# Kernel optimization log

Measured on AMD Instinct MI355X. Metric: run time of the kernel, lower is better.

## Reference

```python
import jax, jax.numpy as jnp
import numpy as np

B, R, NB, T = 32, 96, 5, 2048
FEAT_DIM = 64
SPARSITY = 0.2


def _per_band(X, community, W1, b1, W2, b2):
    # X: [R, T] wavelet coeffs for one (batch, band) slice
    n, t = X.shape
    f32 = X.dtype
    # --- functional connectivity (cosine of centered signals == Pearson corr) ---
    Xc = X - X.mean(axis=1, keepdims=True)
    norm = jnp.linalg.norm(Xc, axis=1, keepdims=True)
    norm = jnp.where(norm == 0, 1.0, norm)
    C = (Xc @ Xc.T) / (norm * norm.T)
    C = jnp.nan_to_num(C, nan=0.0)
    C = C * (1.0 - jnp.eye(n, dtype=f32))  # zero diagonal
    # --- quantile sparsification over strict lower triangle ---
    ti, tj = np.tril_indices(n, -1)
    thr = jnp.quantile(jnp.abs(C[ti, tj]), 1.0 - SPARSITY)
    A = C * (jnp.abs(C) >= thr).astype(f32)  # graph_type == 'weighted'
    # --- node features (5-dim, averaged over regions) ---
    mean_f = X.mean(axis=1)
    std_f = jnp.std(X, axis=1, ddof=1)  # torch.std is unbiased
    energy_f = (X ** 2).sum(axis=1)
    maxamp_f = jnp.abs(X).max(axis=1)
    ps = jnp.abs(jnp.fft.fft(X, axis=1)) ** 2
    ps = ps[:, : t // 2]
    s = ps.sum(axis=1, keepdims=True)
    s = jnp.where(s == 0, 1.0, s)
    p = ps / s
    ent_f = -(p * jnp.log(p + 1e-10)).sum(axis=1)
    node5 = jnp.stack([mean_f, std_f, energy_f, maxamp_f, ent_f], axis=1).mean(axis=0)
    # --- graph properties (6-dim) on binarized adjacency ---
    Bm = (A != 0).astype(f32)
    ne = Bm.sum() / 2.0
    density = ne / (n * (n - 1) / 2.0)
    deg = Bm.sum(axis=1)
    avg_deg = deg.mean()
    A2 = Bm @ Bm
    tri = (A2 * Bm).sum() / 6.0
    poss = (deg * (deg - 1.0)).sum() / 2.0
    clus = jnp.where(poss > 0, tri / jnp.where(poss > 0, poss, 1.0), 0.0)
    # global efficiency: safe reciprocal (zero where A+I == 0; original would emit inf)
    denom = Bm + jnp.eye(n, dtype=f32)
    eff = jnp.where(denom > 0, 1.0 / jnp.where(denom > 0, denom, 1.0), 0.0).sum() / (n * (n - 1))
    # approximate modularity with fixed 2-community assignment (deterministic)
    m2 = 2.0 * ne
    m2_safe = jnp.where(m2 > 0, m2, 1.0)
    same = (community[:, None] == community[None, :]) & (~jnp.eye(n, dtype=bool))
    expected = jnp.outer(deg, deg) / m2_safe
    mod = jnp.where(m2 > 0, (same * (Bm - expected)).sum() / m2_safe, 0.0)
    props = jnp.stack([ne, density, avg_deg, clus, eff, mod])
    feat11 = jnp.concatenate([node5, props])  # [11]
    # --- feature encoder MLP (dropout is identity at inference) ---
    h = jnp.maximum(feat11 @ W1.T + b1, 0.0)
    return A, h @ W2.T + b2


def _forward(wavelet_coeffs, frequency_bands, community, W1, b1, W2, b2):
    b, r, nb, t = wavelet_coeffs.shape
    Xs = wavelet_coeffs.transpose(0, 2, 1, 3).reshape(b * nb, r, t)  # [B*NB, R, T]
    A, F = jax.vmap(_per_band, in_axes=(0, None, None, None, None, None))(
        Xs, community, W1, b1, W2, b2)
    return A.reshape(b, nb, r, r), F.reshape(b, nb, -1)


def setup_inputs() -> dict:
    key = jax.random.key(0)
    k0, k1, k2, k3, k4 = jax.random.split(key, 5)
    wavelet_coeffs = jax.random.normal(k0, (B, R, NB, T), dtype=jnp.float32)
    frequency_bands = jax.random.uniform(k1, (NB, 2), dtype=jnp.float32)
    community = jax.random.randint(k2, (R,), 0, 2)
    W1 = jax.random.normal(k3, (32, 11), dtype=jnp.float32) * 0.3
    b1 = jnp.zeros((32,), jnp.float32)
    W2 = jax.random.normal(k4, (FEAT_DIM, 32), dtype=jnp.float32) * 0.18
    b2 = jnp.zeros((FEAT_DIM,), jnp.float32)
    return {"wavelet_coeffs": wavelet_coeffs, "frequency_bands": frequency_bands,
            "community": community, "W1": W1, "b1": b1, "W2": W2, "b2": b2}


def reference(wavelet_coeffs, frequency_bands, community, W1, b1, W2, b2):
    return _forward(wavelet_coeffs, frequency_bands, community, W1, b1, W2, b2)
```

## Files before the change

kernel.cpp:

```cpp
#include <hip/hip_runtime.h>
#include <hip/hip_bf16.h>
#include <math.h>
#include <float.h>

#ifndef M_PI
#define M_PI 3.14159265358979323846
#endif

#define NBANDS 160
#define RR 96
#define TT 2048
#define NTRIL 4560
#define A_ELEMS ((size_t)NBANDS * RR * RR)
#define NBIN 8192
#define MAXCAND 512
#define BKS 64
#define NST (TT / BKS)
#define GPITCH 76
#define FBLK 384

#define PHI(L) ((L) ^ (((L) >> 5) & 31))

typedef float  f32x4  __attribute__((ext_vector_type(4)));
typedef __bf16 bf16x8 __attribute__((ext_vector_type(8)));
typedef __bf16 bf16x4 __attribute__((ext_vector_type(4)));

__device__ inline void blockReduceSum4(double v0, double v1, double v2, double v3,
                                       double* sred, double out[4]) {
    for (int off = 32; off > 0; off >>= 1) {
        v0 += __shfl_down(v0, off, 64);
        v1 += __shfl_down(v1, off, 64);
        v2 += __shfl_down(v2, off, 64);
        v3 += __shfl_down(v3, off, 64);
    }
    int lane = threadIdx.x & 63, wid = threadIdx.x >> 6;
    int nw = blockDim.x >> 6;
    if (lane == 0) {
        sred[wid * 4 + 0] = v0; sred[wid * 4 + 1] = v1;
        sred[wid * 4 + 2] = v2; sred[wid * 4 + 3] = v3;
    }
    __syncthreads();
    if (threadIdx.x < 4) {
        double r = sred[threadIdx.x];
        for (int w = 1; w < nw; w++) r += sred[w * 4 + threadIdx.x];
        sred[nw * 4 + threadIdx.x] = r;
    }
    __syncthreads();
    out[0] = sred[nw * 4 + 0]; out[1] = sred[nw * 4 + 1];
    out[2] = sred[nw * 4 + 2]; out[3] = sred[nw * 4 + 3];
    __syncthreads();
}

__device__ inline void blockReduceSum2(double v0, double v1,
                                       double* sred, double out[2]) {
    for (int off = 32; off > 0; off >>= 1) {
        v0 += __shfl_down(v0, off, 64);
        v1 += __shfl_down(v1, off, 64);
    }
    int lane = threadIdx.x & 63, wid = threadIdx.x >> 6;
    int nw = blockDim.x >> 6;
    if (lane == 0) { sred[wid * 2 + 0] = v0; sred[wid * 2 + 1] = v1; }
    __syncthreads();
    if (threadIdx.x < 2) {
        double r = sred[threadIdx.x];
        for (int w = 1; w < nw; w++) r += sred[w * 2 + threadIdx.x];
        sred[nw * 2 + threadIdx.x] = r;
    }
    __syncthreads();
    out[0] = sred[nw * 2 + 0]; out[1] = sred[nw * 2 + 1];
    __syncthreads();
}

__device__ inline void blockReduceMax2(double v0, double v1,
                                       double* sred, double out[2]) {
    for (int off = 32; off > 0; off >>= 1) {
        v0 = fmax(v0, __shfl_down(v0, off, 64));
        v1 = fmax(v1, __shfl_down(v1, off, 64));
    }
    int lane = threadIdx.x & 63, wid = threadIdx.x >> 6;
    int nw = blockDim.x >> 6;
    if (lane == 0) { sred[wid * 2 + 0] = v0; sred[wid * 2 + 1] = v1; }
    __syncthreads();
    if (threadIdx.x < 2) {
        double r = sred[threadIdx.x];
        for (int w = 1; w < nw; w++) r = fmax(r, sred[w * 2 + threadIdx.x]);
        sred[nw * 2 + threadIdx.x] = r;
    }
    __syncthreads();
    out[0] = sred[nw * 2 + 0]; out[1] = sred[nw * 2 + 1];
    __syncthreads();
}

__global__ void twiddle_kernel(float* tw) {
    int k = blockIdx.x * blockDim.x + threadIdx.x;
    if (k < 1024) {
        double ang = -2.0 * M_PI * (double)k / 2048.0;
        tw[2 * k]     = (float)cos(ang);
        tw[2 * k + 1] = (float)sin(ang);
    }
}

#define BFLY(r1, r2, WR, WI) do { \
    float _wr = (WR), _wi = (WI); \
    float _tr = _wr * yr[r2] - _wi * yi[r2]; \
    float _ti = _wr * yi[r2] + _wi * yr[r2]; \
    yr[r2] = yr[r1] - _tr; yi[r2] = yi[r1] - _ti; \
    yr[r1] += _tr; yi[r1] += _ti; } while (0)

__global__ __launch_bounds__(256) void rowstat_fft_kernel(
    const float* __restrict__ wc, const float* __restrict__ tw,
    double* __restrict__ rowstats)
{
    __shared__ float re[TT];
    __shared__ float im[TT];
    __shared__ double sred[32];
    __shared__ float bcast[4];

    int t = threadIdx.x;
    int g0 = blockIdx.x * 2;
    int g1 = g0 + 1;

    int band = g0 / RR, r0 = g0 % RR;
    int b = band / 5, nb = band % 5;
    size_t base0 = ((size_t)(b * RR + r0) * 5 + nb) * TT;
    size_t base1 = base0 + (size_t)5 * TT;
    const float2* twv = (const float2*)tw;

    float s0 = 0.f, s1 = 0.f, q0 = 0.f, q1 = 0.f, m0 = 0.f, m1 = 0.f;
#pragma unroll
    for (int c = 0; c < 8; c++) {
        int i = t + c * 256;
        float af = wc[base0 + i];
        float bf = wc[base1 + i];
        int P = PHI(i);
        re[P] = af; im[P] = bf;
        s0 += af; s1 += bf;
        q0 = fmaf(af, af, q0); q1 = fmaf(bf, bf, q1);
        m0 = fmaxf(m0, fabsf(af)); m1 = fmaxf(m1, fabsf(bf));
    }
    __syncthreads();

    double S4[4], M2[2];
    blockReduceSum4((double)s0, (double)s1, (double)q0, (double)q1, sred, S4);
    blockReduceMax2((double)m0, (double)m1, sred, M2);
    double SUM0 = S4[0], SUM1 = S4[1], SQ0 = S4[2], SQ1 = S4[3];
    double MX0 = M2[0], MX1 = M2[1];

    float yr[8], yi[8];

#pragma unroll
    for (int j = 0; j < 8; j++) {
        int p = 8 * t + j;
        int L = (int)(__brev((unsigned)p) >> 21);
        int P = PHI(L);
        yr[j] = re[P]; yi[j] = im[P];
    }

    const float RC = 0.70710678f;
    BFLY(0, 1, 1.0f, 0.0f); BFLY(2, 3, 1.0f, 0.0f);
    BFLY(4, 5, 1.0f, 0.0f); BFLY(6, 7, 1.0f, 0.0f);
    BFLY(0, 2, 1.0f, 0.0f); BFLY(1, 3, 0.0f, -1.0f);
    BFLY(4, 6, 1.0f, 0.0f); BFLY(5, 7, 0.0f, -1.0f);
    BFLY(0, 4, 1.0f, 0.0f); BFLY(1, 5, RC, -RC);
    BFLY(2, 6, 0.0f, -1.0f); BFLY(3, 7, -RC, -RC);

    __syncthreads();
#pragma unroll
    for (int j = 0; j < 8; j++) {
        int P = PHI(8 * t + j);
        re[P] = yr[j]; im[P] = yi[j];
    }
    __syncthreads();
    int oo = t & 7;
    int bb64 = 4 * ((t >> 3) & 7) + (t >> 6);
#pragma unroll
    for (int k = 0; k < 8; k++) {
        int P = PHI(64 * bb64 + 8 * k + oo);
        yr[k] = re[P]; yi[k] = im[P];
    }

    {
        float2 w0 = twv[oo << 7];
        BFLY(0, 1, w0.x, w0.y); BFLY(2, 3, w0.x, w0.y);
        BFLY(4, 5, w0.x, w0.y); BFLY(6, 7, w0.x, w0.y);
        float2 wa = twv[oo << 6];
        float2 wb = twv[(oo + 8) << 6];
        BFLY(0, 2, wa.x, wa.y); BFLY(1, 3, wb.x, wb.y);
        BFLY(4, 6, wa.x, wa.y); BFLY(5, 7, wb.x, wb.y);
        float2 wc0 = twv[oo << 5], wc1 = twv[(oo + 8) << 5];
        float2 wc2 = twv[(oo + 16) << 5], wc3 = twv[(oo + 24) << 5];
        BFLY(0, 4, wc0.x, wc0.y);
        BFLY(1, 5, wc1.x, wc1.y);
        BFLY(2, 6, wc2.x, wc2.y);
        BFLY(3, 7, wc3.x, wc3.y);
    }

    __syncthreads();
#pragma unroll
    for (int k = 0; k < 8; k++) {
        int P = PHI(64 * bb64 + 8 * k + oo);
        re[P] = yr[k]; im[P] = yi[k];
    }
    __syncthreads();
    int O3 = t & 63, Wq = t >> 6;
#pragma unroll
    for (int s = 0; s < 2; s++) {
        int B3 = Wq + 4 * s;
#pragma unroll
        for (int k = 0; k < 4; k++) {
            int P = PHI(256 * B3 + 64 * k + O3);
            yr[4 * s + k] = re[P]; yi[4 * s + k] = im[P];
        }
    }

    {
        float2 w0 = twv[O3 << 4];
        float2 wa = twv[O3 << 3];
        float2 wb = twv[(O3 + 64) << 3];
        BFLY(0, 1, w0.x, w0.y); BFLY(2, 3, w0.x, w0.y);
        BFLY(4, 5, w0.x, w0.y); BFLY(6, 7, w0.x, w0.y);
        BFLY(0, 2, wa.x, wa.y); BFLY(1, 3, wb.x, wb.y);
        BFLY(4, 6, wa.x, wa.y); BFLY(5, 7, wb.x, wb.y);
    }

    __syncthreads();
#pragma unroll
    for (int s = 0; s < 2; s++) {
        int B3 = Wq + 4 * s;
#pragma unroll
        for (int k = 0; k < 4; k++) {
            int P = PHI(256 * B3 + 64 * k + O3);
            re[P] = yr[4 * s + k]; im[P] = yi[4 * s + k];
        }
    }
    __syncthreads();
#pragma unroll
    for (int k = 0; k < 8; k++) {
        int P = PHI(256 * k + t);
        yr[k] = re[P]; yi[k] = im[P];
    }

    {
        float2 w0 = twv[t << 2];
        float2 wa = twv[t << 1];
        float2 wb = twv[(t + 256) << 1];
        BFLY(0, 1, w0.x, w0.y); BFLY(2, 3, w0.x, w0.y);
        BFLY(4, 5, w0.x, w0.y); BFLY(6, 7, w0.x, w0.y);
        BFLY(0, 2, wa.x, wa.y); BFLY(1, 3, wb.x, wb.y);
        BFLY(4, 6, wa.x, wa.y); BFLY(5, 7, wb.x, wb.y);
        float2 wf0 = twv[t], wf1 = twv[t + 256];
        float2 wf2 = twv[t + 512], wf3 = twv[t + 768];
        BFLY(0, 4, wf0.x, wf0.y);
        BFLY(1, 5, wf1.x, wf1.y);
        BFLY(2, 6, wf2.x, wf2.y);
        BFLY(3, 7, wf3.x, wf3.y);
    }

    __syncthreads();
#pragma unroll
    for (int k = 0; k < 8; k++) {
        int P = PHI(256 * k + t);
        re[P] = yr[k]; im[P] = yi[k];
    }
    __syncthreads();

    float psa[8], psb[8];
#pragma unroll
    for (int k = 0; k < 8; k++) {
        int q = (2048 - t - 256 * k) & 2047;
        int P = PHI(q);
        float prr = re[P], pii = im[P];
        float sr = yr[k] + prr, di = yi[k] - pii;
        float si = yi[k] + pii, dr = yr[k] - prr;
        psa[k] = 0.25f * (sr * sr + di * di);
        psb[k] = 0.25f * (si * si + dr * dr);
    }

    float la = 0.f, lb = 0.f;
#pragma unroll
    for (int k = 0; k < 8; k++) { la += psa[k]; lb += psb[k]; }
    double SS[2];
    blockReduceSum2((double)la, (double)lb, sred, SS);
    double SAall = SS[0], SBall = SS[1];
    if (t == 0) {
        bcast[0] = psa[0]; bcast[1] = psa[4];
        bcast[2] = psb[0]; bcast[3] = psb[4];
    }
    __syncthreads();
    double Sa = 0.5 * (SAall + (double)bcast[0] - (double)bcast[1]);
    double Sb = 0.5 * (SBall + (double)bcast[2] - (double)bcast[3]);
    if (Sa == 0.0) Sa = 1.0;
    if (Sb == 0.0) Sb = 1.0;
    float invSa = (float)(1.0 / Sa), invSb = (float)(1.0 / Sb);

    float ea = 0.f, eb = 0.f;
#pragma unroll
    for (int k = 0; k < 8; k++) {
        float pa = psa[k] * invSa;
        float pb = psb[k] * invSb;
        ea += pa * __logf(pa + 1e-10f);
        eb += pb * __logf(pb + 1e-10f);
    }
    double EE[2];
    blockReduceSum2((double)ea, (double)eb, sred, EE);
    double EAall = EE[0], EBall = EE[1];

    if (t == 0) {
        float pa0 = psa[0] * invSa, pa4 = psa[4] * invSa;
        float pb0 = psb[0] * invSb, pb4 = psb[4] * invSb;
        double TA = 0.5 * (EAall + (double)(pa0 * __logf(pa0 + 1e-10f))
                                 - (double)(pa4 * __logf(pa4 + 1e-10f)));
        double TB = 0.5 * (EBall + (double)(pb0 * __logf(pb0 + 1e-10f))
                                 - (double)(pb4 * __logf(pb4 + 1e-10f)));
        double mean0 = SUM0 / (double)TT;
        double mean1 = SUM1 / (double)TT;
        double nsq0 = SQ0 - (double)TT * mean0 * mean0; if (nsq0 < 0) nsq0 = 0;
        double nsq1 = SQ1 - (double)TT * mean1 * mean1; if (nsq1 < 0) nsq1 = 0;
        double* w0 = rowstats + (size_t)g0 * 6;
        double* w1 = rowstats + (size_t)g1 * 6;
        double n0 = sqrt(nsq0), n1 = sqrt(nsq1);
        w0[0] = mean0; w0[1] = (n0 == 0.0 ? 1.0 : n0); w0[2] = sqrt(nsq0 / 2047.0);
        w0[3] = SQ0;   w0[4] = MX0;                    w0[5] = -TA;
        w1[0] = mean1; w1[1] = (n1 == 0.0 ? 1.0 : n1); w1[2] = sqrt(nsq1 / 2047.0);
        w1[3] = SQ1;   w1[4] = MX1;                    w1[5] = -TB;
    }
}

#define CVW(BUF, v, row, c4) do { \
    __bf16 _h0 = (__bf16)v.x, _h1 = (__bf16)v.y, _h2 = (__bf16)v.z, _h3 = (__bf16)v.w; \
    __bf16 _l0 = (__bf16)(v.x - (float)_h0), _l1 = (__bf16)(v.y - (float)_h1); \
    __bf16 _l2 = (__bf16)(v.z - (float)_h2), _l3 = (__bf16)(v.w - (float)_h3); \
    *(bf16x4*)&sh_hi[BUF][row][(c4) * 4] = (bf16x4){_h0, _h1, _h2, _h3}; \
    *(bf16x4*)&sh_lo[BUF][row][(c4) * 4] = (bf16x4){_l0, _l1, _l2, _l3}; } while (0)

#define LDFRAG(dst, arr, BUF, row, ko) do { \
    bf16x4 _f0 = *(const bf16x4*)&arr[BUF][row][ko]; \
    bf16x4 _f1 = *(const bf16x4*)&arr[BUF][row][(ko) + 4]; \
    dst = (bf16x8){_f0[0], _f0[1], _f0[2], _f0[3], _f1[0], _f1[1], _f1[2], _f1[3]}; } while (0)

__global__ __launch_bounds__(FBLK) void fused_gram_finalize_kernel(
    const float* __restrict__ wc, const double* __restrict__ rowstats,
    const int* __restrict__ community,
    const float* __restrict__ W1, const float* __restrict__ b1,
    const float* __restrict__ W2, const float* __restrict__ b2,
    float* __restrict__ A_out, float* __restrict__ F_out)
{
    __shared__ __attribute__((aligned(16))) __bf16 sh_hi[2][RR][GPITCH];
    __shared__ __attribute__((aligned(16))) __bf16 sh_lo[2][RR][GPITCH];
    __shared__ float Cs[RR][RR];
    __shared__ int hist[NBIN];
    __shared__ int chunkv[256];
    __shared__ int pchunk[256];
    __shared__ int gpre_s[64];
    __shared__ float cand[MAXCAND];
    __shared__ int ctrl[8];
    __shared__ float selv[2];
    __shared__ double mean_s[RR], inv_s[RR];
    __shared__ int comm_s[RR];
    __shared__ unsigned long long msk[RR][2];
    __shared__ int deg[RR];
    __shared__ double sred[32];
    __shared__ double feat[11];
    __shared__ double hmlp[32];
    __shared__ double thr_s;

    int band = blockIdx.x, t = threadIdx.x;
    int b = band / 5, nb = band % 5;
    size_t bandbase = ((size_t)b * RR * 5 + nb) * TT;
    const double* rsb = rowstats + (size_t)band * RR * 6;

    if (t < RR) {
        mean_s[t] = rsb[t * 6 + 0];
        inv_s[t]  = 1.0 / rsb[t * 6 + 1];
        comm_s[t] = community[t];
    }
    for (int i = t; i < NBIN; i += FBLK) hist[i] = 0;
    if (t == 0) ctrl[3] = 0;

    int wave = t >> 6, lane = t & 63;
    int m16 = lane & 15, quad = lane >> 4;
    int wr = wave >> 1;
    int wcx = wave & 1;

    int row0 = t >> 4,           c40 = t & 15;
    int row1 = (t + 384) >> 4,   c41 = (t + 384) & 15;
    int row2 = (t + 768) >> 4,   c42 = (t + 768) & 15;
    int row3 = (t + 1152) >> 4,  c43 = (t + 1152) & 15;
    const float* p0 = wc + bandbase + (size_t)row0 * (5 * TT) + c40 * 4;
    const float* p1 = wc + bandbase + (size_t)row1 * (5 * TT) + c41 * 4;
    const float* p2 = wc + bandbase + (size_t)row2 * (5 * TT) + c42 * 4;
    const float* p3 = wc + bandbase + (size_t)row3 * (5 * TT) + c43 * 4;

    f32x4 acc[2][3];
#pragma unroll
    for (int rs = 0; rs < 2; rs++)
#pragma unroll
        for (int cs = 0; cs < 3; cs++) acc[rs][cs] = (f32x4){0.f, 0.f, 0.f, 0.f};

    {
        float4 v0 = *(const float4*)(p0);
        float4 v1 = *(const float4*)(p1);
        float4 v2 = *(const float4*)(p2);
        float4 v3 = *(const float4*)(p3);
        CVW(0, v0, row0, c40); CVW(0, v1, row1, c41);
        CVW(0, v2, row2, c42); CVW(0, v3, row3, c43);
    }
    __syncthreads();

    for (int st = 0; st < NST; st++) {
        int cur = st & 1;
        float4 q0, q1, q2, q3;
        bool more = (st + 1 < NST);
        if (more) {
            int k0 = (st + 1) * BKS;
            q0 = *(const float4*)(p0 + k0);
            q1 = *(const float4*)(p1 + k0);
            q2 = *(const float4*)(p2 + k0);
            q3 = *(const float4*)(p3 + k0);
        }
#pragma unroll
        for (int ks = 0; ks < BKS / 32; ks++) {
            int ko = ks * 32 + quad * 8;
            bf16x8 ah[2], al[2];
#pragma unroll
            for (int rs = 0; rs < 2; rs++) {
                int ar = (wr * 2 + rs) * 16 + m16;
                LDFRAG(ah[rs], sh_hi, cur, ar, ko);
                LDFRAG(al[rs], sh_lo, cur, ar, ko);
            }
#pragma unroll
            for (int cs = 0; cs < 3; cs++) {
                int br = (wcx * 3 + cs) * 16 + m16;
                bf16x8 bh, bl;
                LDFRAG(bh, sh_hi, cur, br, ko);
                LDFRAG(bl, sh_lo, cur, br, ko);
#pragma unroll
                for (int rs = 0; rs < 2; rs++) {
                    acc[rs][cs] = __builtin_amdgcn_mfma_f32_16x16x32_bf16(ah[rs], bh, acc[rs][cs], 0, 0, 0);
                    acc[rs][cs] = __builtin_amdgcn_mfma_f32_16x16x32_bf16(ah[rs], bl, acc[rs][cs], 0, 0, 0);
                    acc[rs][cs] = __builtin_amdgcn_mfma_f32_16x16x32_bf16(al[rs], bh, acc[rs][cs], 0, 0, 0);
                }
            }
        }
        if (more) {
            int nxt = cur ^ 1;
            CVW(nxt, q0, row0, c40); CVW(nxt, q1, row1, c41);
            CVW(nxt, q2, row2, c42); CVW(nxt, q3, row3, c43);
        }
        __syncthreads();
    }

#pragma unroll
    for (int rs = 0; rs < 2; rs++) {
#pragma unroll
        for (int cs = 0; cs < 3; cs++) {
#pragma unroll
            for (int r = 0; r < 4; r++) {
                int grow = (wr * 2 + rs) * 16 + quad * 4 + r;
                int gcol = (wcx * 3 + cs) * 16 + m16;
                double cd = ((double)acc[rs][cs][r]
                             - (double)TT * mean_s[grow] * mean_s[gcol])
                            * (inv_s[grow] * inv_s[gcol]);
                if (grow == gcol) cd = 0.0;
                float cf = (float)cd;
                Cs[grow][gcol] = cf;
                if (gcol < grow) {
                    float val = fabsf(cf);
                    int bin = (int)(val * (float)NBIN);
                    bin = bin > (NBIN - 1) ? (NBIN - 1) : bin;
                    atomicAdd(&hist[bin], 1);
                }
            }
        }
    }
    __syncthreads();

    if (t < 256) {
        int cs = 0;
#pragma unroll
        for (int i = 0; i < NBIN / 256; i++) cs += hist[t * (NBIN / 256) + i];
        chunkv[t] = cs;
    }
    __syncthreads();
    if (t < 64) {
        int s4 = chunkv[4 * t] + chunkv[4 * t + 1] + chunkv[4 * t + 2] + chunkv[4 * t + 3];
        int inc = s4;
        for (int d = 1; d < 64; d <<= 1) {
            int u = __shfl_up(inc, d, 64);
            if (t >= d) inc += u;
        }
        gpre_s[t] = inc - s4;
    }
    __syncthreads();
    if (t < 256) {
        int base = gpre_s[t >> 2];
        for (int j = (t & ~3); j < t; j++) base += chunkv[j];
        pchunk[t] = base;
    }
    __syncthreads();
    if (t < 256) {
        int lo = pchunk[t], hi2 = lo + chunkv[t];
        if (lo <= 3647 && 3647 < hi2) ctrl[4] = t;
        if (lo <= 3648 && 3648 < hi2) ctrl[5] = t;
    }
    __syncthreads();
    {
        int c0 = ctrl[4], c1 = ctrl[5];
        if (t < 32) {
            int binb = c0 * 32;
            int pre = pchunk[c0];
            for (int j = 0; j < t; j++) pre += hist[binb + j];
            int cnt = hist[binb + t];
            if (pre <= 3647 && 3647 < pre + cnt) { ctrl[0] = binb + t; ctrl[2] = pre; }
        } else if (t < 64) {
            int tt2 = t - 32;
            int binb = c1 * 32;
            int pre = pchunk[c1];
            for (int j = 0; j < tt2; j++) pre += hist[binb + j];
            int cnt = hist[binb + tt2];
            if (pre <= 3648 && 3648 < pre + cnt) ctrl[1] = binb + tt2;
        }
    }
    __syncthreads();

    int B0 = ctrl[0], B1 = ctrl[1];
    for (int idx = t; idx < RR * RR; idx += FBLK) {
        int i = idx / RR, j = idx % RR;
        if (j < i) {
            float val = fabsf(Cs[i][j]);
            int bin = (int)(val * (float)NBIN);
            bin = bin > (NBIN - 1) ? (NBIN - 1) : bin;
            if (bin >= B0 && bin <= B1) {
                int k = atomicAdd(&ctrl[3], 1);
                if (k < MAXCAND) cand[k] = val;
            }
        }
    }
    __syncthreads();

    {
        int n = ctrl[3]; if (n > MAXCAND) n = MAXCAND;
        int r0l = 3647 - ctrl[2];
        int r1l = 3648 - ctrl[2];
        for (int i = t; i < n; i += FBLK) {
            float v = cand[i];
            int rank = 0;
            for (int j = 0; j < n; j++) {
                float u = cand[j];
                rank += (u < v || (u == v && j < i)) ? 1 : 0;
            }
            if (rank == r0l) selv[0] = v;
            if (rank == r1l) selv[1] = v;
        }
    }
    __syncthreads();
    if (t == 0) {
        double v0 = (double)selv[0], v1 = (double)selv[1];
        thr_s = v0 + 0.2 * (v1 - v0);
    }
    __syncthreads();
    double thr = thr_s;

    float* Ab = A_out + (size_t)band * (RR * RR);
    for (int idx = t; idx < RR * RR; idx += FBLK) {
        float cf = Cs[idx / RR][idx % RR];
        bool keep = ((double)fabsf(cf) >= thr);
        Ab[idx] = keep ? cf : 0.f;
    }

    for (int i = wave; i < RR; i += 6) {
        float vlo = Cs[i][lane];
        bool klo = ((double)fabsf(vlo) >= thr) && (vlo != 0.f);
        unsigned long long blo = __ballot(klo);
        float vhi = Cs[i][64 + (lane & 31)];
        bool khi = (lane < 32) && ((double)fabsf(vhi) >= thr) && (vhi != 0.f);
        unsigned long long bhi = __ballot(khi) & 0xffffffffull;
        if (lane == 0) {
            msk[i][0] = blo; msk[i][1] = bhi;
            deg[i] = __popcll(blo) + __popcll(bhi);
        }
    }
    __syncthreads();

    double triord = 0, ein = 0, expin = 0;
    for (int idx = t; idx < RR * RR; idx += FBLK) {
        int i = idx / RR, j = idx % RR;
        unsigned long long mi0 = msk[i][0], mi1 = msk[i][1];
        bool bij = (((j < 64) ? (mi0 >> j) : (mi1 >> (j - 64))) & 1ull) != 0;
        if (bij)
            triord += (double)(__popcll(mi0 & msk[j][0]) +
                               __popcll(mi1 & msk[j][1]));
        if (i != j && comm_s[i] == comm_s[j]) {
            ein += bij ? 1.0 : 0.0;
            expin += (double)deg[i] * (double)deg[j];
        }
    }
    double dv = (t < RR) ? (double)deg[t] : 0.0;
    double R1v[4], R2v[4], R3v[2];
    blockReduceSum4(triord, ein, expin, dv, sred, R1v);
    blockReduceSum4((t < RR) ? dv * (dv - 1.0) : 0.0,
                    (t < RR) ? rsb[t * 6 + 0] : 0.0,
                    (t < RR) ? rsb[t * 6 + 2] : 0.0,
                    (t < RR) ? rsb[t * 6 + 3] : 0.0, sred, R2v);
    blockReduceSum2((t < RR) ? rsb[t * 6 + 4] : 0.0,
                    (t < RR) ? rsb[t * 6 + 5] : 0.0, sred, R3v);
    double TRI = R1v[0], EIN = R1v[1], EXPIN = R1v[2], DEGS = R1v[3];
    double POSS2 = R2v[0], N0 = R2v[1], N1 = R2v[2], N2 = R2v[3];
    double N3 = R3v[0], N4 = R3v[1];

    if (t == 0) {
        double ne = 0.5 * DEGS;
        feat[0] = N0 / (double)RR;
        feat[1] = N1 / (double)RR;
        feat[2] = N2 / (double)RR;
        feat[3] = N3 / (double)RR;
        feat[4] = N4 / (double)RR;
        feat[5] = ne;
        feat[6] = ne / (double)NTRIL;
        feat[7] = DEGS / (double)RR;
        double tri = TRI / 6.0, poss = POSS2 * 0.5;
        feat[8] = (poss > 0.0) ? tri / poss : 0.0;
        feat[9] = ((double)RR + DEGS) / ((double)RR * (double)(RR - 1));
        double m2 = DEGS;
        feat[10] = (m2 > 0.0) ? (EIN - EXPIN / m2) / m2 : 0.0;
    }
    __syncthreads();

    if (t < 32) {
        double a = (double)b1[t];
        for (int k = 0; k < 11; k++) a += (double)W1[t * 11 + k] * feat[k];
        hmlp[t] = (a > 0.0) ? a : 0.0;
    }
    __syncthreads();
    if (t < 64) {
        double a = (double)b2[t];
        for (int j = 0; j < 32; j++) a += (double)W2[t * 32 + j] * hmlp[j];
        F_out[(size_t)band * 64 + t] = (float)a;
    }
}

extern "C" void kernel_launch(void* const* d_in, const int* in_sizes, int n_in,
                              void* d_out, int out_size, void* d_ws, size_t ws_size,
                              hipStream_t stream) {
    const float* wc        = (const float*)d_in[0];
    const int*   community = (const int*)d_in[2];
    const float* W1        = (const float*)d_in[3];
    const float* b1        = (const float*)d_in[4];
    const float* W2        = (const float*)d_in[5];
    const float* b2        = (const float*)d_in[6];

    float* A_out = (float*)d_out;
    float* F_out = A_out + A_ELEMS;

    char* ws = (char*)d_ws;
    float*  tw       = (float*)ws;
    double* rowstats = (double*)(ws + 8192);

    hipLaunchKernelGGL(twiddle_kernel, dim3(4), dim3(256), 0, stream, tw);
    hipLaunchKernelGGL(rowstat_fft_kernel, dim3(NBANDS * RR / 2), dim3(256), 0, stream,
                       wc, tw, rowstats);
    hipLaunchKernelGGL(fused_gram_finalize_kernel, dim3(NBANDS), dim3(FBLK), 0, stream,
                       wc, rowstats, community, W1, b1, W2, b2, A_out, F_out);
}
```

Before: 294.7 us.

## Split Gram computation over K into separate kernel, then reduce in finalize

Splits the fused per-band Gram plus finalize kernel in two. A split-K Gram kernel launches 4x more blocks, each covering a quarter of the time axis and writing partial 96x96 sums to workspace. A 256-thread finalize kernel then sums the partials and does the correlation, histogram-quantile and graph-property work. The aim is to fill the GPU's compute units, since 160 blocks underfill it, at the cost of an extra launch and a global round trip for the partial matrices.

```diff
diff --git a/kernel.cpp b/kernel.cpp
--- a/kernel.cpp
+++ b/kernel.cpp
@@ -15,9 +15,12 @@
 #define NBIN 8192
 #define MAXCAND 512
 #define BKS 64
-#define NST (TT / BKS)
+#define KSPLIT 4
+#define KCH (TT / KSPLIT)
+#define GSTAGES (KCH / BKS)
 #define GPITCH 76
-#define FBLK 384
+#define GRAM_BLK 384
+#define FIN_BLK 256
 
 #define PHI(L) ((L) ^ (((L) >> 5) & 31))
 
@@ -338,15 +341,112 @@
     bf16x4 _f1 = *(const bf16x4*)&arr[BUF][row][(ko) + 4]; \
     dst = (bf16x8){_f0[0], _f0[1], _f0[2], _f0[3], _f1[0], _f1[1], _f1[2], _f1[3]}; } while (0)
 
-__global__ __launch_bounds__(FBLK) void fused_gram_finalize_kernel(
-    const float* __restrict__ wc, const double* __restrict__ rowstats,
+__global__ __launch_bounds__(GRAM_BLK) void gram_part_kernel(
+    const float* __restrict__ wc, float* __restrict__ Gpart)
+{
+    __shared__ __attribute__((aligned(16))) __bf16 sh_hi[2][RR][GPITCH];
+    __shared__ __attribute__((aligned(16))) __bf16 sh_lo[2][RR][GPITCH];
+
+    int bid = blockIdx.x, t = threadIdx.x;
+    int band = bid / KSPLIT, kc = bid % KSPLIT;
+    int b = band / 5, nb = band % 5;
+    size_t bandbase = ((size_t)b * RR * 5 + nb) * TT + (size_t)kc * KCH;
+
+    int wave = t >> 6, lane = t & 63;
+    int m16 = lane & 15, quad = lane >> 4;
+    int wr = wave >> 1;
+    int wcx = wave & 1;
+
+    int row0 = t >> 4,           c40 = t & 15;
+    int row1 = (t + 384) >> 4,   c41 = (t + 384) & 15;
+    int row2 = (t + 768) >> 4,   c42 = (t + 768) & 15;
+    int row3 = (t + 1152) >> 4,  c43 = (t + 1152) & 15;
+    const float* p0 = wc + bandbase + (size_t)row0 * (5 * TT) + c40 * 4;
+    const float* p1 = wc + bandbase + (size_t)row1 * (5 * TT) + c41 * 4;
+    const float* p2 = wc + bandbase + (size_t)row2 * (5 * TT) + c42 * 4;
+    const float* p3 = wc + bandbase + (size_t)row3 * (5 * TT) + c43 * 4;
+
+    f32x4 acc[2][3];
+#pragma unroll
+    for (int rs = 0; rs < 2; rs++)
+#pragma unroll
+        for (int cs = 0; cs < 3; cs++) acc[rs][cs] = (f32x4){0.f, 0.f, 0.f, 0.f};
+
+    {
+        float4 v0 = *(const float4*)(p0);
+        float4 v1 = *(const float4*)(p1);
+        float4 v2 = *(const float4*)(p2);
+        float4 v3 = *(const float4*)(p3);
+        CVW(0, v0, row0, c40); CVW(0, v1, row1, c41);
+        CVW(0, v2, row2, c42); CVW(0, v3, row3, c43);
+    }
+    __syncthreads();
+
+    for (int st = 0; st < GSTAGES; st++) {
+        int cur = st & 1;
+        float4 q0, q1, q2, q3;
+        bool more = (st + 1 < GSTAGES);
+        if (more) {
+            int k0 = (st + 1) * BKS;
+            q0 = *(const float4*)(p0 + k0);
+            q1 = *(const float4*)(p1 + k0);
+            q2 = *(const float4*)(p2 + k0);
+            q3 = *(const float4*)(p3 + k0);
+        }
+#pragma unroll
+        for (int ks = 0; ks < BKS / 32; ks++) {
+            int ko = ks * 32 + quad * 8;
+            bf16x8 ah[2], al[2];
+#pragma unroll
+            for (int rs = 0; rs < 2; rs++) {
+                int ar = (wr * 2 + rs) * 16 + m16;
+                LDFRAG(ah[rs], sh_hi, cur, ar, ko);
+                LDFRAG(al[rs], sh_lo, cur, ar, ko);
+            }
+#pragma unroll
+            for (int cs = 0; cs < 3; cs++) {
+                int br = (wcx * 3 + cs) * 16 + m16;
+                bf16x8 bh, bl;
+                LDFRAG(bh, sh_hi, cur, br, ko);
+                LDFRAG(bl, sh_lo, cur, br, ko);
+#pragma unroll
+                for (int rs = 0; rs < 2; rs++) {
+                    acc[rs][cs] = __builtin_amdgcn_mfma_f32_16x16x32_bf16(ah[rs], bh, acc[rs][cs], 0, 0, 0);
+                    acc[rs][cs] = __builtin_amdgcn_mfma_f32_16x16x32_bf16(ah[rs], bl, acc[rs][cs], 0, 0, 0);
+                    acc[rs][cs] = __builtin_amdgcn_mfma_f32_16x16x32_bf16(al[rs], bh, acc[rs][cs], 0, 0, 0);
+                }
+            }
+        }
+        if (more) {
+            int nxt = cur ^ 1;
+            CVW(nxt, q0, row0, c40); CVW(nxt, q1, row1, c41);
+            CVW(nxt, q2, row2, c42); CVW(nxt, q3, row3, c43);
+        }
+        __syncthreads();
+    }
+
+    float* Gp = Gpart + (size_t)bid * (RR * RR);
+#pragma unroll
+    for (int rs = 0; rs < 2; rs++) {
+#pragma unroll
+        for (int cs = 0; cs < 3; cs++) {
+#pragma unroll
+            for (int r = 0; r < 4; r++) {
+                int grow = (wr * 2 + rs) * 16 + quad * 4 + r;
+                int gcol = (wcx * 3 + cs) * 16 + m16;
+                Gp[grow * RR + gcol] = acc[rs][cs][r];
+            }
+        }
+    }
+}
+
+__global__ __launch_bounds__(FIN_BLK) void band_finalize_kernel(
+    const float* __restrict__ Gpart, const double* __restrict__ rowstats,
     const int* __restrict__ community,
     const float* __restrict__ W1, const float* __restrict__ b1,
     const float* __restrict__ W2, const float* __restrict__ b2,
     float* __restrict__ A_out, float* __restrict__ F_out)
 {
-    __shared__ __attribute__((aligned(16))) __bf16 sh_hi[2][RR][GPITCH];
-    __shared__ __attribute__((aligned(16))) __bf16 sh_lo[2][RR][GPITCH];
     __shared__ float Cs[RR][RR];
     __shared__ int hist[NBIN];
     __shared__ int chunkv[256];
@@ -365,8 +465,6 @@
     __shared__ double thr_s;
 
     int band = blockIdx.x, t = threadIdx.x;
-    int b = band / 5, nb = band % 5;
-    size_t bandbase = ((size_t)b * RR * 5 + nb) * TT;
     const double* rsb = rowstats + (size_t)band * RR * 6;
 
     if (t < RR) {
@@ -374,108 +472,31 @@
         inv_s[t]  = 1.0 / rsb[t * 6 + 1];
         comm_s[t] = community[t];
     }
-    for (int i = t; i < NBIN; i += FBLK) hist[i] = 0;
+    for (int i = t; i < NBIN; i += FIN_BLK) hist[i] = 0;
     if (t == 0) ctrl[3] = 0;
-
-    int wave = t >> 6, lane = t & 63;
-    int m16 = lane & 15, quad = lane >> 4;
-    int wr = wave >> 1;
-    int wcx = wave & 1;
-
-    int row0 = t >> 4,           c40 = t & 15;
-    int row1 = (t + 384) >> 4,   c41 = (t + 384) & 15;
-    int row2 = (t + 768) >> 4,   c42 = (t + 768) & 15;
-    int row3 = (t + 1152) >> 4,  c43 = (t + 1152) & 15;
-    const float* p0 = wc + bandbase + (size_t)row0 * (5 * TT) + c40 * 4;
-    const float* p1 = wc + bandbase + (size_t)row1 * (5 * TT) + c41 * 4;
-    const float* p2 = wc + bandbase + (size_t)row2 * (5 * TT) + c42 * 4;
-    const float* p3 = wc + bandbase + (size_t)row3 * (5 * TT) + c43 * 4;
-
-    f32x4 acc[2][3];
-#pragma unroll
-    for (int rs = 0; rs < 2; rs++)
-#pragma unroll
-        for (int cs = 0; cs < 3; cs++) acc[rs][cs] = (f32x4){0.f, 0.f, 0.f, 0.f};
-
-    {
-        float4 v0 = *(const float4*)(p0);
-        float4 v1 = *(const float4*)(p1);
-        float4 v2 = *(const float4*)(p2);
-        float4 v3 = *(const float4*)(p3);
-        CVW(0, v0, row0, c40); CVW(0, v1, row1, c41);
-        CVW(0, v2, row2, c42); CVW(0, v3, row3, c43);
-    }
-    __syncthreads();
-
-    for (int st = 0; st < NST; st++) {
-        int cur = st & 1;
-        float4 q0, q1, q2, q3;
-        bool more = (st + 1 < NST);
-        if (more) {
-            int k0 = (st + 1) * BKS;
-            q0 = *(const float4*)(p0 + k0);
-            q1 = *(const float4*)(p1 + k0);
-            q2 = *(const float4*)(p2 + k0);
-            q3 = *(const float4*)(p3 + k0);
-        }
-#pragma unroll
-        for (int ks = 0; ks < BKS / 32; ks++) {
-            int ko = ks * 32 + quad * 8;
-            bf16x8 ah[2], al[2];
-#pragma unroll
-            for (int rs = 0; rs < 2; rs++) {
-                int ar = (wr * 2 + rs) * 16 + m16;
-                LDFRAG(ah[rs], sh_hi, cur, ar, ko);
-                LDFRAG(al[rs], sh_lo, cur, ar, ko);
-            }
-#pragma unroll
-            for (int cs = 0; cs < 3; cs++) {
-                int br = (wcx * 3 + cs) * 16 + m16;
-                bf16x8 bh, bl;
-                LDFRAG(bh, sh_hi, cur, br, ko);
-                LDFRAG(bl, sh_lo, cur, br, ko);
-#pragma unroll
-                for (int rs = 0; rs < 2; rs++) {
-                    acc[rs][cs] = __builtin_amdgcn_mfma_f32_16x16x32_bf16(ah[rs], bh, acc[rs][cs], 0, 0, 0);
-                    acc[rs][cs] = __builtin_amdgcn_mfma_f32_16x16x32_bf16(ah[rs], bl, acc[rs][cs], 0, 0, 0);
-                    acc[rs][cs] = __builtin_amdgcn_mfma_f32_16x16x32_bf16(al[rs], bh, acc[rs][cs], 0, 0, 0);
-                }
-            }
-        }
-        if (more) {
-            int nxt = cur ^ 1;
-            CVW(nxt, q0, row0, c40); CVW(nxt, q1, row1, c41);
-            CVW(nxt, q2, row2, c42); CVW(nxt, q3, row3, c43);
-        }
-        __syncthreads();
-    }
-
-#pragma unroll
-    for (int rs = 0; rs < 2; rs++) {
-#pragma unroll
-        for (int cs = 0; cs < 3; cs++) {
-#pragma unroll
-            for (int r = 0; r < 4; r++) {
-                int grow = (wr * 2 + rs) * 16 + quad * 4 + r;
-                int gcol = (wcx * 3 + cs) * 16 + m16;
-                double cd = ((double)acc[rs][cs][r]
-                             - (double)TT * mean_s[grow] * mean_s[gcol])
-                            * (inv_s[grow] * inv_s[gcol]);
-                if (grow == gcol) cd = 0.0;
-                float cf = (float)cd;
-                Cs[grow][gcol] = cf;
-                if (gcol < grow) {
-                    float val = fabsf(cf);
-                    int bin = (int)(val * (float)NBIN);
-                    bin = bin > (NBIN - 1) ? (NBIN - 1) : bin;
-                    atomicAdd(&hist[bin], 1);
-                }
-            }
-        }
-    }
-    __syncthreads();
-
-    if (t < 256) {
+    __syncthreads();
+
+    const float* Pb = Gpart + (size_t)band * KSPLIT * (RR * RR);
+    for (int idx = t; idx < RR * RR; idx += FIN_BLK) {
+        float g = 0.f;
+#pragma unroll
+        for (int c = 0; c < KSPLIT; c++) g += Pb[(size_t)c * (RR * RR) + idx];
+        int i = idx / RR, j = idx % RR;
+        double cd = ((double)g - (double)TT * mean_s[i] * mean_s[j])
+                    * (inv_s[i] * inv_s[j]);
+        if (i == j) cd = 0.0;
+        float cf = (float)cd;
+        Cs[i][j] = cf;
+        if (j < i) {
+            float val = fabsf(cf);
+            int bin = (int)(val * (float)NBIN);
+            bin = bin > (NBIN - 1) ? (NBIN - 1) : bin;
+            atomicAdd(&hist[bin], 1);
+        }
+    }
+    __syncthreads();
+
+    {
         int cs = 0;
 #pragma unroll
         for (int i = 0; i < NBIN / 256; i++) cs += hist[t * (NBIN / 256) + i];
@@ -492,13 +513,13 @@
         gpre_s[t] = inc - s4;
     }
     __syncthreads();
-    if (t < 256) {
+    {
         int base = gpre_s[t >> 2];
         for (int j = (t & ~3); j < t; j++) base += chunkv[j];
         pchunk[t] = base;
     }
     __syncthreads();
-    if (t < 256) {
+    {
         int lo = pchunk[t], hi2 = lo + chunkv[t];
         if (lo <= 3647 && 3647 < hi2) ctrl[4] = t;
         if (lo <= 3648 && 3648 < hi2) ctrl[5] = t;
@@ -524,7 +545,7 @@
     __syncthreads();
 
     int B0 = ctrl[0], B1 = ctrl[1];
-    for (int idx = t; idx < RR * RR; idx += FBLK) {
+    for (int idx = t; idx < RR * RR; idx += FIN_BLK) {
         int i = idx / RR, j = idx % RR;
         if (j < i) {
             float val = fabsf(Cs[i][j]);
@@ -542,7 +563,7 @@
         int n = ctrl[3]; if (n > MAXCAND) n = MAXCAND;
         int r0l = 3647 - ctrl[2];
         int r1l = 3648 - ctrl[2];
-        for (int i = t; i < n; i += FBLK) {
+        for (int i = t; i < n; i += FIN_BLK) {
             float v = cand[i];
             int rank = 0;
             for (int j = 0; j < n; j++) {
@@ -562,13 +583,14 @@
     double thr = thr_s;
 
     float* Ab = A_out + (size_t)band * (RR * RR);
-    for (int idx = t; idx < RR * RR; idx += FBLK) {
+    for (int idx = t; idx < RR * RR; idx += FIN_BLK) {
         float cf = Cs[idx / RR][idx % RR];
         bool keep = ((double)fabsf(cf) >= thr);
         Ab[idx] = keep ? cf : 0.f;
     }
 
-    for (int i = wave; i < RR; i += 6) {
+    int wave = t >> 6, lane = t & 63;
+    for (int i = wave; i < RR; i += 4) {
         float vlo = Cs[i][lane];
         bool klo = ((double)fabsf(vlo) >= thr) && (vlo != 0.f);
         unsigned long long blo = __ballot(klo);
@@ -583,7 +605,7 @@
     __syncthreads();
 
     double triord = 0, ein = 0, expin = 0;
-    for (int idx = t; idx < RR * RR; idx += FBLK) {
+    for (int idx = t; idx < RR * RR; idx += FIN_BLK) {
         int i = idx / RR, j = idx % RR;
         unsigned long long mi0 = msk[i][0], mi1 = msk[i][1];
         bool bij = (((j < 64) ? (mi0 >> j) : (mi1 >> (j - 64))) & 1ull) != 0;
@@ -655,10 +677,13 @@
     char* ws = (char*)d_ws;
     float*  tw       = (float*)ws;
     double* rowstats = (double*)(ws + 8192);
+    float*  Gpart    = (float*)(ws + 745472);
 
     hipLaunchKernelGGL(twiddle_kernel, dim3(4), dim3(256), 0, stream, tw);
     hipLaunchKernelGGL(rowstat_fft_kernel, dim3(NBANDS * RR / 2), dim3(256), 0, stream,
                        wc, tw, rowstats);
-    hipLaunchKernelGGL(fused_gram_finalize_kernel, dim3(NBANDS), dim3(FBLK), 0, stream,
-                       wc, rowstats, community, W1, b1, W2, b2, A_out, F_out);
-}
+    hipLaunchKernelGGL(gram_part_kernel, dim3(NBANDS * KSPLIT), dim3(GRAM_BLK), 0, stream,
+                       wc, Gpart);
+    hipLaunchKernelGGL(band_finalize_kernel, dim3(NBANDS), dim3(FIN_BLK), 0, stream,
+                       Gpart, rowstats, community, W1, b1, W2, b2, A_out, F_out);
+}
```

Measured after the change: 308.3 us. 4.6% more time.
